# Performance work log

Measured on AMD Instinct MI355X. Metric: run time of the kernel, lower is better.

Reference implementation:

```python
import jax, jax.numpy as jnp
import numpy as np

B, L, D, K, O, DM = 32, 512, 32, 6, 192, 512
Q = 0.75
EPS = 1e-6
BN_EPS = 1e-5


def _torch_median(a, axis):
    # torch.median returns the LOWER of the two middle values for even n
    n = a.shape[axis]
    s = jnp.sort(a, axis=axis)
    return jnp.take(s, jnp.array([(n - 1) // 2]), axis=axis)


def setup_inputs() -> dict:
    key = jax.random.key(0)
    ks = jax.random.split(key, 5)
    return {
        "x": jax.random.normal(ks[0], (B, L, D), jnp.float32),
        "x_date": jax.random.normal(ks[1], (B, L, D, K), jnp.float32),
        "y_date": jax.random.normal(ks[2], (B, O, D, K), jnp.float32),
        "mlp_w1": jax.random.normal(ks[3], (L, DM), jnp.float32) * 0.02,
        "mlp_b1": jnp.zeros((DM,), jnp.float32),
        "mlp_w2": jax.random.normal(ks[4], (DM, 2), jnp.float32) * 0.02,
        "mlp_b2": jnp.zeros((2,), jnp.float32),
        "bn_gamma": jnp.ones((D,), jnp.float32),
        "bn_beta": jnp.zeros((D,), jnp.float32),
    }


def reference(x, x_date, y_date, mlp_w1, mlp_b1, mlp_w2, mlp_b2, bn_gamma, bn_beta):
    k = x_date.shape[-1]
    # robust location/scale (median + interquantile range), reduced over time dim 1
    med_true = _torch_median(x, 1)                 # (B,1,D)
    med_map = _torch_median(x_date, 1)             # (B,1,D,K)
    std_true = (jnp.quantile(x, Q, axis=1, keepdims=True)
                - jnp.quantile(x, 1.0 - Q, axis=1, keepdims=True) + EPS)   # (B,1,D)
    std_map = (jnp.quantile(x_date, Q, axis=1, keepdims=True)
               - jnp.quantile(x_date, 1.0 - Q, axis=1, keepdims=True) + EPS)  # (B,1,D,K)
    x_date_map = (x_date - med_map) / std_map * std_true[..., None] + med_true[..., None]
    y_date_map = (y_date - med_map) / std_map * std_true[..., None] + med_true[..., None]

    # cross-attention over time with tiny contraction dim k
    scores = jnp.einsum('bldk,bodk->bdlo', x_date_map, y_date_map)  # (B,D,L,O)
    A = jax.nn.softmax(scores / jnp.sqrt(jnp.float32(k)), axis=-2)  # softmax over L
    V = jnp.einsum('bld,bdlo->bdo', x, A)                           # (B,D,O)

    # BatchNorm1d(d_feature) in training mode: batch stats over (B, O); dropout = identity (eval)
    mu = jnp.mean(V, axis=(0, 2), keepdims=True)
    var = jnp.var(V, axis=(0, 2), keepdims=True)
    y = (V - mu) * jax.lax.rsqrt(var + BN_EPS) * bn_gamma[None, :, None] + bn_beta[None, :, None]
    y = jnp.transpose(y, (0, 2, 1))                                 # (B,O,D)

    # softmax-gated fusion MLP over the time axis
    error = x - x_date_map.mean(-1)                                 # (B,L,D)
    h = jax.nn.gelu(jnp.einsum('bld,lm->bdm', error, mlp_w1) + mlp_b1, approximate=False)
    w = jax.nn.softmax(h @ mlp_w2 + mlp_b2, axis=-1)                # (B,D,2)

    y_map = jnp.stack([y_date_map.mean(-1), y], axis=-1)            # (B,O,D,2)
    pred = jnp.sum(y_map * w[:, None], axis=-1)                     # (B,O,D)
    return pred
```

## Files before the change

### kernel.cpp

```cpp
#include <hip/hip_runtime.h>
#include <math.h>

#define BB 32
#define LL 512
#define DD 32
#define KK 6
#define OO 192
#define DM 512

typedef __fp16 h2 __attribute__((ext_vector_type(2)));
typedef __fp16 h8 __attribute__((ext_vector_type(8)));
union F2H { float f; h2 h; };
__device__ __forceinline__ float asF(h2 h) { F2H u; u.h = h; return u.f; }
__device__ __forceinline__ h2 asH(float f) { F2H u; u.f = f; return u.h; }

typedef short bf16x8 __attribute__((ext_vector_type(8)));
typedef float f4 __attribute__((ext_vector_type(4)));
union U16x8 { uint4 u; bf16x8 h; };
union UH8F { uint4 u; h8 h; };

__device__ __forceinline__ unsigned short f2bf(float x) {
  unsigned int u = __float_as_uint(x);
  u = (u + 0x7FFF + ((u >> 16) & 1)) >> 16;
  return (unsigned short)u;
}

#define MOVDPP(x, ctrl) \
  __int_as_float(__builtin_amdgcn_mov_dpp(__float_as_int(x), ctrl, 0xf, 0xf, true))

#define CSTR2 524
#define XD0   0
#define XV0   6288
#define MEDO  7336
#define STDO  7350
#define SAO   7364
#define SCO   7376
#define BNR   7388
#define XMP   0
#define YMP   4096
#define DEN   7404
#define NUM   8172
#define LDSF  8940

__device__ __forceinline__ void sort512(float v[8], int lane) {
  #pragma unroll
  for (int k = 2; k <= 512; k <<= 1) {
    #pragma unroll
    for (int j = k >> 1; j > 0; j >>= 1) {
      if (j >= 8) {
        int jj = j >> 3;
        bool lower = (lane & jj) == 0;
        bool asc = ((lane << 3) & k) == 0;
        bool keepmin = (asc == lower);
        #pragma unroll
        for (int r = 0; r < 8; ++r) {
          float o;
          if (jj == 1)      o = MOVDPP(v[r], 0xB1);
          else if (jj == 2) o = MOVDPP(v[r], 0x4E);
          else if (jj == 8) o = MOVDPP(v[r], 0x128);
          else              o = __shfl_xor(v[r], jj);
          v[r] = keepmin ? fminf(v[r], o) : fmaxf(v[r], o);
        }
      } else {
        #pragma unroll
        for (int r = 0; r < 8; ++r) {
          if ((r & j) == 0) {
            int r2 = r | j;
            bool asc = (((lane << 3) | r) & k) == 0;
            float a = v[r], b = v[r2];
            float lo = fminf(a, b), hi = fmaxf(a, b);
            v[r]  = asc ? lo : hi;
            v[r2] = asc ? hi : lo;
          }
        }
      }
    }
  }
}

__global__ __launch_bounds__(512, 4) void fused_kernel(
    const float* __restrict__ x, const float* __restrict__ x_date,
    const float* __restrict__ y_date, const float* __restrict__ w1,
    float* __restrict__ V, float* __restrict__ ymean,
    float* __restrict__ bnp, unsigned short* __restrict__ errb,
    unsigned short* __restrict__ w1t) {
  __shared__ float lds[LDSF];
  int orig = blockIdx.x;
  int tid = threadIdx.x, lane = tid & 63, wv = tid >> 6;

  if (orig >= 512) {
    float* tw = lds;
    int id = orig - 512;
    int l0 = (id & 7) * 64, m0 = (id >> 3) * 64;
    #pragma unroll
    for (int it = 0; it < 2; ++it) {
      int f = tid + it * 512;
      int row = f >> 4, c4 = f & 15;
      float4 v = ((const float4*)(w1 + (size_t)(l0 + row) * DM + m0))[c4];
      float* p = &tw[row * 68 + c4 * 4];
      p[0] = v.x; p[1] = v.y; p[2] = v.z; p[3] = v.w;
    }
    __syncthreads();
    unsigned int* w1t32 = (unsigned int*)w1t;
    #pragma unroll
    for (int it = 0; it < 4; ++it) {
      int f = tid + it * 512;
      int mr = f >> 5, c = f & 31;
      float a = tw[(c * 2 + 0) * 68 + mr];
      float b = tw[(c * 2 + 1) * 68 + mr];
      unsigned int u = (unsigned int)f2bf(a) | ((unsigned int)f2bf(b) << 16);
      w1t32[(size_t)(m0 + mr) * (DM / 2) + (l0 >> 1) + c] = u;
    }
    return;
  }

  int xcd = orig & 7, idx = orig >> 3;
  int b = (xcd << 2) | (idx >> 4);
  int d0 = (idx & 15) << 1;

  const float* xs = x_date + (size_t)b * LL * 192 + d0 * 6;
  #pragma unroll
  for (int it = 0; it < 3; ++it) {
    int f = tid + it * 512;
    int row = f / 3, c4 = f % 3;
    float4 v = ((const float4*)(xs + (size_t)row * 192))[c4];
    int col = c4 * 4;
    lds[XD0 + (col + 0) * CSTR2 + row] = v.x;
    lds[XD0 + (col + 1) * CSTR2 + row] = v.y;
    lds[XD0 + (col + 2) * CSTR2 + row] = v.z;
    lds[XD0 + (col + 3) * CSTR2 + row] = v.w;
  }
  {
    int row = tid;
    float2 v = *(const float2*)(x + (size_t)(b * LL + row) * DD + d0);
    lds[XV0 + row]         = v.x;
    lds[XV0 + CSTR2 + row] = v.y;
  }

  float2 yr[3][3];
  if ((wv & 3) == 0) {
    int dme = d0 + (wv >> 2);
    #pragma unroll
    for (int j = 0; j < 3; ++j) {
      const float2* yp = (const float2*)(
          y_date + (((size_t)b * OO + (lane + 64 * j)) * DD + dme) * KK);
      yr[j][0] = yp[0]; yr[j][1] = yp[1]; yr[j][2] = yp[2];
    }
  }
  __syncthreads();

  for (int p = 0; p < 2; ++p) {
    int s = p * 8 + wv;
    if (s < 14) {
      const float4* colp = (s < 12)
          ? (const float4*)&lds[XD0 + s * CSTR2 + lane * 8]
          : (const float4*)&lds[XV0 + (s - 12) * CSTR2 + lane * 8];
      float v[8];
      float4 c0 = colp[0], c1 = colp[1];
      v[0]=c0.x; v[1]=c0.y; v[2]=c0.z; v[3]=c0.w;
      v[4]=c1.x; v[5]=c1.y; v[6]=c1.z; v[7]=c1.w;
      sort512(v, lane);
      float e127 = __shfl(v[7], 15);
      float e128 = __shfl(v[0], 16);
      float e255 = __shfl(v[7], 31);
      float e383 = __shfl(v[7], 47);
      float e384 = __shfl(v[0], 48);
      if (lane == 0) {
        float q25 = e127 + 0.75f * (e128 - e127);
        float q75 = e383 + 0.25f * (e384 - e383);
        lds[MEDO + s] = e255;
        lds[STDO + s] = q75 - q25 + 1e-6f;
      }
    }
  }
  __syncthreads();

  if (tid < 12) {
    int dloc = tid / 6;
    float a = lds[STDO + 12 + dloc] / lds[STDO + tid];
    lds[SAO + tid] = a;
    lds[SCO + tid] = lds[MEDO + 12 + dloc] - lds[MEDO + tid] * a;
  }
  __syncthreads();

  const float PSC = 0.58912435f;

  float4 packed[2];
  {
    int l = tid;
    #pragma unroll
    for (int dli = 0; dli < 2; ++dli) {
      int cb = dli * 6;
      float m0 = lds[SAO+cb+0] * lds[XD0 + (cb + 0) * CSTR2 + l] + lds[SCO+cb+0];
      float m1 = lds[SAO+cb+1] * lds[XD0 + (cb + 1) * CSTR2 + l] + lds[SCO+cb+1];
      float m2 = lds[SAO+cb+2] * lds[XD0 + (cb + 2) * CSTR2 + l] + lds[SCO+cb+2];
      float m3 = lds[SAO+cb+3] * lds[XD0 + (cb + 3) * CSTR2 + l] + lds[SCO+cb+3];
      float m4 = lds[SAO+cb+4] * lds[XD0 + (cb + 4) * CSTR2 + l] + lds[SCO+cb+4];
      float m5 = lds[SAO+cb+5] * lds[XD0 + (cb + 5) * CSTR2 + l] + lds[SCO+cb+5];
      float xvv = lds[XV0 + dli * CSTR2 + l];
      errb[(size_t)((b << 5) | (d0 + dli)) * LL + l] =
          f2bf(xvv - (m0 + m1 + m2 + m3 + m4 + m5) * (1.0f / 6.0f));
      packed[dli].x = asF(__builtin_amdgcn_cvt_pkrtz(m0 * PSC, m1 * PSC));
      packed[dli].y = asF(__builtin_amdgcn_cvt_pkrtz(m2 * PSC, m3 * PSC));
      packed[dli].z = asF(__builtin_amdgcn_cvt_pkrtz(m4 * PSC, m5 * PSC));
      packed[dli].w = 0.0f;
    }
  }
  __syncthreads();

  *(float4*)&lds[XMP + (0 * 512 + tid) * 4] = packed[0];
  *(float4*)&lds[XMP + (1 * 512 + tid) * 4] = packed[1];
  if ((wv & 3) == 0) {
    int dl = wv >> 2, dme = d0 + dl;
    float askw[6], cskw[6];
    #pragma unroll
    for (int k = 0; k < 6; ++k) {
      askw[k] = lds[SAO + dl * 6 + k];
      cskw[k] = lds[SCO + dl * 6 + k];
    }
    #pragma unroll
    for (int j = 0; j < 3; ++j) {
      int o = lane + 64 * j;
      float q0 = askw[0] * yr[j][0].x + cskw[0];
      float q1 = askw[1] * yr[j][0].y + cskw[1];
      float q2 = askw[2] * yr[j][1].x + cskw[2];
      float q3 = askw[3] * yr[j][1].y + cskw[3];
      float q4 = askw[4] * yr[j][2].x + cskw[4];
      float q5 = askw[5] * yr[j][2].y + cskw[5];
      ymean[(size_t)((b << 5) | dme) * OO + o] =
          (q0 + q1 + q2 + q3 + q4 + q5) * (1.0f / 6.0f);
      float4 yq;
      yq.x = asF(__builtin_amdgcn_cvt_pkrtz(q0, q1));
      yq.y = asF(__builtin_amdgcn_cvt_pkrtz(q2, q3));
      yq.z = asF(__builtin_amdgcn_cvt_pkrtz(q4, q5));
      yq.w = 0.0f;
      *(float4*)&lds[YMP + (dl * 192 + o) * 4] = yq;
    }
  }
  __syncthreads();

  {
    int adl = wv >> 2, oh = (wv >> 1) & 1, lh = wv & 1;
    int l15 = lane & 15, kg = lane >> 4;
    uint4 zero4 = make_uint4(0u, 0u, 0u, 0u);

    UH8F bf[6];
    #pragma unroll
    for (int ot = 0; ot < 6; ++ot) {
      int brow = (oh * 6 + ot) * 16 + l15;
      uint4 bu = *(const uint4*)&lds[YMP + (adl * 192 + brow) * 4];
      bf[ot].u = (kg == 0) ? bu : zero4;
    }

    float den[6] = {0.f,0.f,0.f,0.f,0.f,0.f};
    float num[6] = {0.f,0.f,0.f,0.f,0.f,0.f};

    for (int t = 0; t < 16; ++t) {
      int lt = lh * 16 + t;
      UH8F af;
      uint4 au = *(const uint4*)&lds[XMP + (adl * 512 + lt * 16 + l15) * 4];
      af.u = (kg == 0) ? au : zero4;
      int rbase = lt * 16 + kg * 4;
      float xv0 = lds[XV0 + adl * CSTR2 + rbase + 0];
      float xv1 = lds[XV0 + adl * CSTR2 + rbase + 1];
      float xv2 = lds[XV0 + adl * CSTR2 + rbase + 2];
      float xv3 = lds[XV0 + adl * CSTR2 + rbase + 3];
      #pragma unroll
      for (int ot = 0; ot < 6; ++ot) {
        f4 c = __builtin_amdgcn_mfma_f32_16x16x32_f16(
            af.h, bf[ot].h, (f4){0.f, 0.f, 0.f, 0.f}, 0, 0, 0);
        float e0 = exp2f(c[0]), e1 = exp2f(c[1]);
        float e2 = exp2f(c[2]), e3 = exp2f(c[3]);
        den[ot] += (e0 + e1) + (e2 + e3);
        num[ot] += (e0 * xv0 + e1 * xv1) + (e2 * xv2 + e3 * xv3);
      }
    }

    #pragma unroll
    for (int ot = 0; ot < 6; ++ot) {
      den[ot] += __shfl_xor(den[ot], 16);
      den[ot] += __shfl_xor(den[ot], 32);
      num[ot] += __shfl_xor(num[ot], 16);
      num[ot] += __shfl_xor(num[ot], 32);
    }
    if (lane < 16) {
      #pragma unroll
      for (int ot = 0; ot < 6; ++ot) {
        lds[DEN + wv * 96 + ot * 16 + lane] = den[ot];
        lds[NUM + wv * 96 + ot * 16 + lane] = num[ot];
      }
    }
  }
  __syncthreads();

  float s1 = 0.f, s2 = 0.f;
  if (tid < 384) {
    int dl2 = tid / 192, o = tid % 192;
    int oh2 = o / 96, r96 = o % 96;
    int wv0 = dl2 * 4 + oh2 * 2;
    float dsum = lds[DEN + wv0 * 96 + r96] + lds[DEN + (wv0 + 1) * 96 + r96];
    float nsum = lds[NUM + wv0 * 96 + r96] + lds[NUM + (wv0 + 1) * 96 + r96];
    float vv = nsum / dsum;
    V[(size_t)((b << 5) | (d0 + dl2)) * OO + o] = vv;
    s1 = vv; s2 = vv * vv;
  }
  #pragma unroll
  for (int off = 32; off > 0; off >>= 1) {
    s1 += __shfl_down(s1, off);
    s2 += __shfl_down(s2, off);
  }
  if (lane == 0) { lds[BNR + wv] = s1; lds[BNR + 8 + wv] = s2; }
  __syncthreads();
  if (tid == 0) {
    float S0  = lds[BNR + 0] + lds[BNR + 1] + lds[BNR + 2];
    float S20 = lds[BNR + 8] + lds[BNR + 9] + lds[BNR + 10];
    float S1  = lds[BNR + 3] + lds[BNR + 4] + lds[BNR + 5];
    float S21 = lds[BNR + 11] + lds[BNR + 12] + lds[BNR + 13];
    bnp[(d0 << 5) | b]                = S0;
    bnp[1024 + ((d0 << 5) | b)]       = S20;
    bnp[((d0 + 1) << 5) | b]          = S1;
    bnp[1024 + (((d0 + 1) << 5) | b)] = S21;
  }
}

__global__ __launch_bounds__(256) void gate_kernel(
    const unsigned short* __restrict__ errb, const unsigned short* __restrict__ w1t,
    const float* __restrict__ b1, const float* __restrict__ w2,
    float* __restrict__ gatep) {
  __shared__ float part[4][32];
  int orig = blockIdx.x;
  int xcd = orig & 7, idx = orig >> 3;
  int b = (xcd << 2) | (idx >> 3);
  int s = idx & 7;
  int tid = threadIdx.x, lane = tid & 63, wv = tid >> 6;
  int m16 = lane & 15, quad = lane >> 4;
  int mw = s * 64 + wv * 16;
  int r0 = b * 32;

  float b1v = b1[mw + m16];
  float2 w2p = ((const float2*)w2)[mw + m16];
  float w2d = w2p.x - w2p.y;

  f4 acc[2];
  acc[0] = (f4){0.f, 0.f, 0.f, 0.f};
  acc[1] = (f4){0.f, 0.f, 0.f, 0.f};

  const unsigned short* ea = errb + (size_t)(r0 + m16) * DM + quad * 8;
  const unsigned short* eb = ea + 16 * DM;
  const unsigned short* wb = w1t + (size_t)(mw + m16) * DM + quad * 8;

  #pragma unroll
  for (int ks = 0; ks < DM; ks += 32) {
    U16x8 ua0, ua1, ub;
    ua0.u = *(const uint4*)(ea + ks);
    ua1.u = *(const uint4*)(eb + ks);
    ub.u  = *(const uint4*)(wb + ks);
    acc[0] = __builtin_amdgcn_mfma_f32_16x16x32_bf16(ua0.h, ub.h, acc[0], 0, 0, 0);
    acc[1] = __builtin_amdgcn_mfma_f32_16x16x32_bf16(ua1.h, ub.h, acc[1], 0, 0, 0);
  }

  float rsum[2][4];
  #pragma unroll
  for (int rt = 0; rt < 2; ++rt) {
    #pragma unroll
    for (int r = 0; r < 4; ++r) {
      float h = acc[rt][r] + b1v;
      float gg = 0.5f * h * (1.0f + erff(h * 0.70710678f));
      rsum[rt][r] = gg * w2d;
    }
  }
  #pragma unroll
  for (int rt = 0; rt < 2; ++rt) {
    #pragma unroll
    for (int r = 0; r < 4; ++r) {
      rsum[rt][r] += __shfl_xor(rsum[rt][r], 1);
      rsum[rt][r] += __shfl_xor(rsum[rt][r], 2);
      rsum[rt][r] += __shfl_xor(rsum[rt][r], 4);
      rsum[rt][r] += __shfl_xor(rsum[rt][r], 8);
    }
  }
  if (m16 == 0) {
    #pragma unroll
    for (int rt = 0; rt < 2; ++rt)
      #pragma unroll
      for (int r = 0; r < 4; ++r)
        part[wv][rt * 16 + quad * 4 + r] = rsum[rt][r];
  }
  __syncthreads();

  if (tid < 32) {
    float p = part[0][tid] + part[1][tid] + part[2][tid] + part[3][tid];
    gatep[(size_t)(((b << 3) | s) << 5) | tid] = p;
  }
}

__global__ __launch_bounds__(256) void tail_kernel(
    const float* __restrict__ gatep, const float* __restrict__ b2,
    const float* __restrict__ V, const float* __restrict__ ymean,
    const float* __restrict__ bnp,
    const float* __restrict__ gamma, const float* __restrict__ beta,
    float* __restrict__ out) {
  __shared__ float vsh[32 * 28], ysh[32 * 28];
  __shared__ float gsh[32], ssh[32], osh[32];
  int g = blockIdx.x, tid = threadIdx.x;
  int xcd = g & 7, idx = g >> 3;
  int b = (xcd << 2) | (idx >> 3);
  int o0 = (idx & 7) * 24;

  if (tid < 192) {
    int dd = tid / 6, c4 = tid % 6;
    size_t goff = (size_t)(b * DD + dd) * OO + o0;
    float4 v = ((const float4*)(V + goff))[c4];
    float4 y = ((const float4*)(ymean + goff))[c4];
    *(float4*)&vsh[dd * 28 + c4 * 4] = v;
    *(float4*)&ysh[dd * 28 + c4 * 4] = y;
  }

  if (tid < 32) {
    float ld = b2[0] - b2[1];
    #pragma unroll
    for (int s = 0; s < 8; ++s)
      ld += gatep[(size_t)(((b << 3) | s) << 5) | tid];
    gsh[tid] = 1.0f / (1.0f + expf(-ld));
    float S = 0.f, S2 = 0.f;
    const float* pd = bnp + (tid << 5);
    #pragma unroll 8
    for (int bb = 0; bb < 32; ++bb) { S += pd[bb]; S2 += pd[1024 + bb]; }
    const float inv = 1.0f / (BB * OO);
    float mu = S * inv;
    float var = S2 * inv - mu * mu;
    float gg = gamma[tid] * rsqrtf(var + 1e-5f);
    ssh[tid] = gg;
    osh[tid] = beta[tid] - mu * gg;
  }
  __syncthreads();

  if (tid < 192) {
    int op = tid >> 3, c4 = tid & 7;
    float4 r;
    #pragma unroll
    for (int j = 0; j < 4; ++j) {
      int dd = c4 * 4 + j;
      float v  = vsh[dd * 28 + op];
      float ym = ysh[dd * 28 + op];
      float gg = gsh[dd];
      float y  = v * ssh[dd] + osh[dd];
      ((float*)&r)[j] = ym * gg + y * (1.0f - gg);
    }
    ((float4*)(out + (size_t)(b * OO + o0 + op) * DD))[c4] = r;
  }
}

extern "C" void kernel_launch(void* const* d_in, const int* in_sizes, int n_in,
                              void* d_out, int out_size, void* d_ws, size_t ws_size,
                              hipStream_t stream) {
  const float* x      = (const float*)d_in[0];
  const float* x_date = (const float*)d_in[1];
  const float* y_date = (const float*)d_in[2];
  const float* w1     = (const float*)d_in[3];
  const float* b1     = (const float*)d_in[4];
  const float* w2     = (const float*)d_in[5];
  const float* b2     = (const float*)d_in[6];
  const float* gamma  = (const float*)d_in[7];
  const float* beta   = (const float*)d_in[8];
  float* out = (float*)d_out;

  float* ws    = (float*)d_ws;
  float* V     = ws;
  float* ymean = ws + 196608;
  float* bnp   = ws + 393216;
  unsigned short* errb = (unsigned short*)(ws + 395264);
  unsigned short* w1t  = (unsigned short*)(ws + 657408);
  float* gatep = ws + 788480;

  fused_kernel<<<576, 512, 0, stream>>>(x, x_date, y_date, w1,
                                        V, ymean, bnp, errb, w1t);
  gate_kernel<<<256, 256, 0, stream>>>(errb, w1t, b1, w2, gatep);
  tail_kernel<<<256, 256, 0, stream>>>(gatep, b2, V, ymean, bnp,
                                       gamma, beta, out);
}
```

Baseline: 138.3 us.

## Split fused kernel to one feature per block for more parallelism

Each block of the fused kernel now handles a single (batch, feature) pair instead of two, doubling the grid to 1024 work blocks plus the weight-transpose blocks. LDS use is roughly halved, and the launch bound is raised to 8 blocks per CU for higher occupancy. The attention loop now splits the time dimension across four waves per output half instead of two, and the partial sums are combined with four-way adds. The aim is to spread the sort and MFMA work across more CUs and hide latency. In exchange, the per-block fixed costs (loads, syncs) are duplicated and only 7 of 8 waves take part in the sort phase.

```diff
diff --git a/kernel.cpp b/kernel.cpp
--- a/kernel.cpp
+++ b/kernel.cpp
@@ -30,17 +30,17 @@
 
 #define CSTR2 524
 #define XD0   0
-#define XV0   6288
-#define MEDO  7336
-#define STDO  7350
-#define SAO   7364
-#define SCO   7376
-#define BNR   7388
+#define XV0   3144
+#define MEDO  3668
+#define STDO  3675
+#define SAO   3682
+#define SCO   3688
+#define BNR   3694
 #define XMP   0
-#define YMP   4096
-#define DEN   7404
-#define NUM   8172
-#define LDSF  8940
+#define YMP   2048
+#define DEN   3712
+#define NUM   4480
+#define LDSF  5248
 
 __device__ __forceinline__ void sort512(float v[8], int lane) {
   #pragma unroll
@@ -78,7 +78,7 @@
   }
 }
 
-__global__ __launch_bounds__(512, 4) void fused_kernel(
+__global__ __launch_bounds__(512, 8) void fused_kernel(
     const float* __restrict__ x, const float* __restrict__ x_date,
     const float* __restrict__ y_date, const float* __restrict__ w1,
     float* __restrict__ V, float* __restrict__ ymean,
@@ -88,9 +88,9 @@
   int orig = blockIdx.x;
   int tid = threadIdx.x, lane = tid & 63, wv = tid >> 6;
 
-  if (orig >= 512) {
+  if (orig >= 1024) {
     float* tw = lds;
-    int id = orig - 512;
+    int id = orig - 1024;
     int l0 = (id & 7) * 64, m0 = (id >> 3) * 64;
     #pragma unroll
     for (int it = 0; it < 2; ++it) {
@@ -115,132 +115,103 @@
   }
 
   int xcd = orig & 7, idx = orig >> 3;
-  int b = (xcd << 2) | (idx >> 4);
-  int d0 = (idx & 15) << 1;
-
-  const float* xs = x_date + (size_t)b * LL * 192 + d0 * 6;
+  int b = (xcd << 2) | (idx >> 5);
+  int d = idx & 31;
+  int lbid = (b << 5) | d;
+
+  const float* xs = x_date + (size_t)b * LL * 192 + d * 6;
   #pragma unroll
   for (int it = 0; it < 3; ++it) {
     int f = tid + it * 512;
-    int row = f / 3, c4 = f % 3;
-    float4 v = ((const float4*)(xs + (size_t)row * 192))[c4];
-    int col = c4 * 4;
-    lds[XD0 + (col + 0) * CSTR2 + row] = v.x;
-    lds[XD0 + (col + 1) * CSTR2 + row] = v.y;
-    lds[XD0 + (col + 2) * CSTR2 + row] = v.z;
-    lds[XD0 + (col + 3) * CSTR2 + row] = v.w;
-  }
-  {
-    int row = tid;
-    float2 v = *(const float2*)(x + (size_t)(b * LL + row) * DD + d0);
-    lds[XV0 + row]         = v.x;
-    lds[XV0 + CSTR2 + row] = v.y;
-  }
-
-  float2 yr[3][3];
-  if ((wv & 3) == 0) {
-    int dme = d0 + (wv >> 2);
-    #pragma unroll
-    for (int j = 0; j < 3; ++j) {
-      const float2* yp = (const float2*)(
-          y_date + (((size_t)b * OO + (lane + 64 * j)) * DD + dme) * KK);
-      yr[j][0] = yp[0]; yr[j][1] = yp[1]; yr[j][2] = yp[2];
-    }
-  }
-  __syncthreads();
-
-  for (int p = 0; p < 2; ++p) {
-    int s = p * 8 + wv;
-    if (s < 14) {
-      const float4* colp = (s < 12)
-          ? (const float4*)&lds[XD0 + s * CSTR2 + lane * 8]
-          : (const float4*)&lds[XV0 + (s - 12) * CSTR2 + lane * 8];
-      float v[8];
-      float4 c0 = colp[0], c1 = colp[1];
-      v[0]=c0.x; v[1]=c0.y; v[2]=c0.z; v[3]=c0.w;
-      v[4]=c1.x; v[5]=c1.y; v[6]=c1.z; v[7]=c1.w;
-      sort512(v, lane);
-      float e127 = __shfl(v[7], 15);
-      float e128 = __shfl(v[0], 16);
-      float e255 = __shfl(v[7], 31);
-      float e383 = __shfl(v[7], 47);
-      float e384 = __shfl(v[0], 48);
-      if (lane == 0) {
-        float q25 = e127 + 0.75f * (e128 - e127);
-        float q75 = e383 + 0.25f * (e384 - e383);
-        lds[MEDO + s] = e255;
-        lds[STDO + s] = q75 - q25 + 1e-6f;
-      }
-    }
-  }
-  __syncthreads();
-
-  if (tid < 12) {
-    int dloc = tid / 6;
-    float a = lds[STDO + 12 + dloc] / lds[STDO + tid];
+    int row = f / 3, c = f % 3;
+    float2 v = ((const float2*)(xs + (size_t)row * 192))[c];
+    lds[XD0 + (2 * c + 0) * CSTR2 + row] = v.x;
+    lds[XD0 + (2 * c + 1) * CSTR2 + row] = v.y;
+  }
+  lds[XV0 + tid] = x[(size_t)(b * LL + tid) * DD + d];
+
+  float2 yr0, yr1, yr2;
+  if (wv < 3) {
+    int o = wv * 64 + lane;
+    const float2* yp = (const float2*)(
+        y_date + (((size_t)b * OO + o) * DD + d) * KK);
+    yr0 = yp[0]; yr1 = yp[1]; yr2 = yp[2];
+  }
+  __syncthreads();
+
+  if (wv < 7) {
+    const float4* colp = (wv < 6)
+        ? (const float4*)&lds[XD0 + wv * CSTR2 + lane * 8]
+        : (const float4*)&lds[XV0 + lane * 8];
+    float v[8];
+    float4 c0 = colp[0], c1 = colp[1];
+    v[0]=c0.x; v[1]=c0.y; v[2]=c0.z; v[3]=c0.w;
+    v[4]=c1.x; v[5]=c1.y; v[6]=c1.z; v[7]=c1.w;
+    sort512(v, lane);
+    float e127 = __shfl(v[7], 15);
+    float e128 = __shfl(v[0], 16);
+    float e255 = __shfl(v[7], 31);
+    float e383 = __shfl(v[7], 47);
+    float e384 = __shfl(v[0], 48);
+    if (lane == 0) {
+      float q25 = e127 + 0.75f * (e128 - e127);
+      float q75 = e383 + 0.25f * (e384 - e383);
+      lds[MEDO + wv] = e255;
+      lds[STDO + wv] = q75 - q25 + 1e-6f;
+    }
+  }
+  __syncthreads();
+
+  if (tid < 6) {
+    float a = lds[STDO + 6] / lds[STDO + tid];
     lds[SAO + tid] = a;
-    lds[SCO + tid] = lds[MEDO + 12 + dloc] - lds[MEDO + tid] * a;
+    lds[SCO + tid] = lds[MEDO + 6] - lds[MEDO + tid] * a;
   }
   __syncthreads();
 
   const float PSC = 0.58912435f;
 
-  float4 packed[2];
+  float4 packed;
   {
     int l = tid;
-    #pragma unroll
-    for (int dli = 0; dli < 2; ++dli) {
-      int cb = dli * 6;
-      float m0 = lds[SAO+cb+0] * lds[XD0 + (cb + 0) * CSTR2 + l] + lds[SCO+cb+0];
-      float m1 = lds[SAO+cb+1] * lds[XD0 + (cb + 1) * CSTR2 + l] + lds[SCO+cb+1];
-      float m2 = lds[SAO+cb+2] * lds[XD0 + (cb + 2) * CSTR2 + l] + lds[SCO+cb+2];
-      float m3 = lds[SAO+cb+3] * lds[XD0 + (cb + 3) * CSTR2 + l] + lds[SCO+cb+3];
-      float m4 = lds[SAO+cb+4] * lds[XD0 + (cb + 4) * CSTR2 + l] + lds[SCO+cb+4];
-      float m5 = lds[SAO+cb+5] * lds[XD0 + (cb + 5) * CSTR2 + l] + lds[SCO+cb+5];
-      float xvv = lds[XV0 + dli * CSTR2 + l];
-      errb[(size_t)((b << 5) | (d0 + dli)) * LL + l] =
-          f2bf(xvv - (m0 + m1 + m2 + m3 + m4 + m5) * (1.0f / 6.0f));
-      packed[dli].x = asF(__builtin_amdgcn_cvt_pkrtz(m0 * PSC, m1 * PSC));
-      packed[dli].y = asF(__builtin_amdgcn_cvt_pkrtz(m2 * PSC, m3 * PSC));
-      packed[dli].z = asF(__builtin_amdgcn_cvt_pkrtz(m4 * PSC, m5 * PSC));
-      packed[dli].w = 0.0f;
-    }
-  }
-  __syncthreads();
-
-  *(float4*)&lds[XMP + (0 * 512 + tid) * 4] = packed[0];
-  *(float4*)&lds[XMP + (1 * 512 + tid) * 4] = packed[1];
-  if ((wv & 3) == 0) {
-    int dl = wv >> 2, dme = d0 + dl;
-    float askw[6], cskw[6];
-    #pragma unroll
-    for (int k = 0; k < 6; ++k) {
-      askw[k] = lds[SAO + dl * 6 + k];
-      cskw[k] = lds[SCO + dl * 6 + k];
-    }
-    #pragma unroll
-    for (int j = 0; j < 3; ++j) {
-      int o = lane + 64 * j;
-      float q0 = askw[0] * yr[j][0].x + cskw[0];
-      float q1 = askw[1] * yr[j][0].y + cskw[1];
-      float q2 = askw[2] * yr[j][1].x + cskw[2];
-      float q3 = askw[3] * yr[j][1].y + cskw[3];
-      float q4 = askw[4] * yr[j][2].x + cskw[4];
-      float q5 = askw[5] * yr[j][2].y + cskw[5];
-      ymean[(size_t)((b << 5) | dme) * OO + o] =
-          (q0 + q1 + q2 + q3 + q4 + q5) * (1.0f / 6.0f);
-      float4 yq;
-      yq.x = asF(__builtin_amdgcn_cvt_pkrtz(q0, q1));
-      yq.y = asF(__builtin_amdgcn_cvt_pkrtz(q2, q3));
-      yq.z = asF(__builtin_amdgcn_cvt_pkrtz(q4, q5));
-      yq.w = 0.0f;
-      *(float4*)&lds[YMP + (dl * 192 + o) * 4] = yq;
-    }
+    float m0 = lds[SAO+0] * lds[XD0 + 0 * CSTR2 + l] + lds[SCO+0];
+    float m1 = lds[SAO+1] * lds[XD0 + 1 * CSTR2 + l] + lds[SCO+1];
+    float m2 = lds[SAO+2] * lds[XD0 + 2 * CSTR2 + l] + lds[SCO+2];
+    float m3 = lds[SAO+3] * lds[XD0 + 3 * CSTR2 + l] + lds[SCO+3];
+    float m4 = lds[SAO+4] * lds[XD0 + 4 * CSTR2 + l] + lds[SCO+4];
+    float m5 = lds[SAO+5] * lds[XD0 + 5 * CSTR2 + l] + lds[SCO+5];
+    float xvv = lds[XV0 + l];
+    errb[(size_t)lbid * LL + l] =
+        f2bf(xvv - (m0 + m1 + m2 + m3 + m4 + m5) * (1.0f / 6.0f));
+    packed.x = asF(__builtin_amdgcn_cvt_pkrtz(m0 * PSC, m1 * PSC));
+    packed.y = asF(__builtin_amdgcn_cvt_pkrtz(m2 * PSC, m3 * PSC));
+    packed.z = asF(__builtin_amdgcn_cvt_pkrtz(m4 * PSC, m5 * PSC));
+    packed.w = 0.0f;
+  }
+  __syncthreads();
+
+  *(float4*)&lds[XMP + tid * 4] = packed;
+  if (wv < 3) {
+    int o = wv * 64 + lane;
+    float q0 = lds[SAO+0] * yr0.x + lds[SCO+0];
+    float q1 = lds[SAO+1] * yr0.y + lds[SCO+1];
+    float q2 = lds[SAO+2] * yr1.x + lds[SCO+2];
+    float q3 = lds[SAO+3] * yr1.y + lds[SCO+3];
+    float q4 = lds[SAO+4] * yr2.x + lds[SCO+4];
+    float q5 = lds[SAO+5] * yr2.y + lds[SCO+5];
+    ymean[(size_t)lbid * OO + o] =
+        (q0 + q1 + q2 + q3 + q4 + q5) * (1.0f / 6.0f);
+    float4 yq;
+    yq.x = asF(__builtin_amdgcn_cvt_pkrtz(q0, q1));
+    yq.y = asF(__builtin_amdgcn_cvt_pkrtz(q2, q3));
+    yq.z = asF(__builtin_amdgcn_cvt_pkrtz(q4, q5));
+    yq.w = 0.0f;
+    *(float4*)&lds[YMP + o * 4] = yq;
   }
   __syncthreads();
 
   {
-    int adl = wv >> 2, oh = (wv >> 1) & 1, lh = wv & 1;
+    int oh = wv >> 2, lq = wv & 3;
     int l15 = lane & 15, kg = lane >> 4;
     uint4 zero4 = make_uint4(0u, 0u, 0u, 0u);
 
@@ -248,23 +219,23 @@
     #pragma unroll
     for (int ot = 0; ot < 6; ++ot) {
       int brow = (oh * 6 + ot) * 16 + l15;
-      uint4 bu = *(const uint4*)&lds[YMP + (adl * 192 + brow) * 4];
+      uint4 bu = *(const uint4*)&lds[YMP + brow * 4];
       bf[ot].u = (kg == 0) ? bu : zero4;
     }
 
     float den[6] = {0.f,0.f,0.f,0.f,0.f,0.f};
     float num[6] = {0.f,0.f,0.f,0.f,0.f,0.f};
 
-    for (int t = 0; t < 16; ++t) {
-      int lt = lh * 16 + t;
+    for (int t = 0; t < 8; ++t) {
+      int lt = lq * 8 + t;
       UH8F af;
-      uint4 au = *(const uint4*)&lds[XMP + (adl * 512 + lt * 16 + l15) * 4];
+      uint4 au = *(const uint4*)&lds[XMP + (lt * 16 + l15) * 4];
       af.u = (kg == 0) ? au : zero4;
       int rbase = lt * 16 + kg * 4;
-      float xv0 = lds[XV0 + adl * CSTR2 + rbase + 0];
-      float xv1 = lds[XV0 + adl * CSTR2 + rbase + 1];
-      float xv2 = lds[XV0 + adl * CSTR2 + rbase + 2];
-      float xv3 = lds[XV0 + adl * CSTR2 + rbase + 3];
+      float xv0 = lds[XV0 + rbase + 0];
+      float xv1 = lds[XV0 + rbase + 1];
+      float xv2 = lds[XV0 + rbase + 2];
+      float xv3 = lds[XV0 + rbase + 3];
       #pragma unroll
       for (int ot = 0; ot < 6; ++ot) {
         f4 c = __builtin_amdgcn_mfma_f32_16x16x32_f16(
@@ -294,14 +265,16 @@
   __syncthreads();
 
   float s1 = 0.f, s2 = 0.f;
-  if (tid < 384) {
-    int dl2 = tid / 192, o = tid % 192;
+  if (tid < OO) {
+    int o = tid;
     int oh2 = o / 96, r96 = o % 96;
-    int wv0 = dl2 * 4 + oh2 * 2;
-    float dsum = lds[DEN + wv0 * 96 + r96] + lds[DEN + (wv0 + 1) * 96 + r96];
-    float nsum = lds[NUM + wv0 * 96 + r96] + lds[NUM + (wv0 + 1) * 96 + r96];
+    int w0 = oh2 * 4;
+    float dsum = lds[DEN + (w0 + 0) * 96 + r96] + lds[DEN + (w0 + 1) * 96 + r96]
+               + lds[DEN + (w0 + 2) * 96 + r96] + lds[DEN + (w0 + 3) * 96 + r96];
+    float nsum = lds[NUM + (w0 + 0) * 96 + r96] + lds[NUM + (w0 + 1) * 96 + r96]
+               + lds[NUM + (w0 + 2) * 96 + r96] + lds[NUM + (w0 + 3) * 96 + r96];
     float vv = nsum / dsum;
-    V[(size_t)((b << 5) | (d0 + dl2)) * OO + o] = vv;
+    V[(size_t)lbid * OO + o] = vv;
     s1 = vv; s2 = vv * vv;
   }
   #pragma unroll
@@ -312,14 +285,10 @@
   if (lane == 0) { lds[BNR + wv] = s1; lds[BNR + 8 + wv] = s2; }
   __syncthreads();
   if (tid == 0) {
-    float S0  = lds[BNR + 0] + lds[BNR + 1] + lds[BNR + 2];
-    float S20 = lds[BNR + 8] + lds[BNR + 9] + lds[BNR + 10];
-    float S1  = lds[BNR + 3] + lds[BNR + 4] + lds[BNR + 5];
-    float S21 = lds[BNR + 11] + lds[BNR + 12] + lds[BNR + 13];
-    bnp[(d0 << 5) | b]                = S0;
-    bnp[1024 + ((d0 << 5) | b)]       = S20;
-    bnp[((d0 + 1) << 5) | b]          = S1;
-    bnp[1024 + (((d0 + 1) << 5) | b)] = S21;
+    float S  = lds[BNR + 0] + lds[BNR + 1] + lds[BNR + 2];
+    float S2 = lds[BNR + 8] + lds[BNR + 9] + lds[BNR + 10];
+    bnp[(d << 5) | b]          = S;
+    bnp[1024 + ((d << 5) | b)] = S2;
   }
 }
 
@@ -473,8 +442,8 @@
   unsigned short* w1t  = (unsigned short*)(ws + 657408);
   float* gatep = ws + 788480;
 
-  fused_kernel<<<576, 512, 0, stream>>>(x, x_date, y_date, w1,
-                                        V, ymean, bnp, errb, w1t);
+  fused_kernel<<<1088, 512, 0, stream>>>(x, x_date, y_date, w1,
+                                         V, ymean, bnp, errb, w1t);
   gate_kernel<<<256, 256, 0, stream>>>(errb, w1t, b1, w2, gatep);
   tail_kernel<<<256, 256, 0, stream>>>(gatep, b2, V, ymean, bnp,
                                        gamma, beta, out);
```

After: 133.7 us. -3.3%, faster.
